# Kernel optimization log

Measured on AMD Instinct MI355X. Metric: run time of the kernel, lower is better.

Reference implementation:

```python
import jax, jax.numpy as jnp
import numpy as np

B, S, T, D = 64, 256, 8, 256
E, M = 500000, 2048
NEG_INF = -10000000000.0


def setup_inputs() -> dict:
    key = jax.random.key(0)
    ks = jax.random.split(key, 9)
    token_reprs = jax.random.normal(ks[0], (B, S, T, D), dtype=jnp.float32)
    w1 = jax.random.normal(ks[1], (D, D // 2), dtype=jnp.float32) * (1.0 / np.sqrt(D))
    b1 = jnp.zeros((D // 2,), dtype=jnp.float32)
    w2 = jax.random.normal(ks[2], (D // 2, 1), dtype=jnp.float32) * (1.0 / np.sqrt(D // 2))
    b2 = jnp.zeros((1,), dtype=jnp.float32)
    edge_index = jax.random.randint(ks[3], (2, E), 0, B * S, dtype=jnp.int32)
    lm_indices = jax.random.randint(ks[4], (M,), 0, B * S * T, dtype=jnp.int32)
    batch_pointers = jax.random.randint(ks[5], (M,), 0, B, dtype=jnp.int32)
    tree_padding_mask = jax.random.randint(ks[6], (B, S), 0, 2, dtype=jnp.int32).astype(jnp.bool_)
    return {
        "token_reprs": token_reprs,
        "w1": w1, "b1": b1, "w2": w2, "b2": b2,
        "edge_index": edge_index,
        "lm_indices": lm_indices,
        "batch_pointers": batch_pointers,
        "tree_padding_mask": tree_padding_mask,
    }


def reference(token_reprs, w1, b1, w2, b2, edge_index, lm_indices, batch_pointers, tree_padding_mask):
    b, s, t, d = token_reprs.shape
    # type representation is the first token of each type tree
    type_reprs = token_reprs[:, :, 0]                  # [B, S, D]
    flat_types = type_reprs.reshape(b * s, d)          # [B*S, D]

    # predict_lemmas: gather scope/goal reprs, elementwise multiply, 2-layer MLP
    scope_ids, goal_ids = edge_index[0], edge_index[1]
    h = flat_types[scope_ids] * flat_types[goal_ids]   # [E, D]
    h = h @ w1 + b1                                    # [E, D//2] (Dropout is identity in eval)
    lemmas = (h @ w2 + b2)[:, 0]                       # [E]

    # predict_masks: gather masked token reprs + per-tree candidates, dot, mask
    mask_reprs = token_reprs.reshape(b * s * t, d)[lm_indices]  # [M, D]
    candidates = type_reprs[batch_pointers]            # [M, S, D]
    candidate_mask = tree_padding_mask[batch_pointers] # [M, S]
    lm_preds = jnp.einsum('md,msd->ms', mask_reprs, candidates)
    lm_preds = jnp.where(candidate_mask, lm_preds, NEG_INF)
    return lemmas, lm_preds
```

## Files before the change

kernel.cpp:

```cpp
#include <hip/hip_runtime.h>

#define DD 256
#define SS 256
#define BB 64
#define NEDGE 500000
#define MM 2048
#define NEG_INF -10000000000.0f
#define ROWF4 512
#define NROWS (BB * SS)

#define OFF_VC     0
#define OFF_MSORT  4096
#define OFF_BSTART (4096 + MM * 4)
#define OFF_ASLAB  (1 << 16)
#define OFF_P2     ((1 << 16) + (8 << 20))
#define OFF_MROWS  ((1 << 16) + (16 << 20))

__device__ __forceinline__ float bflo(unsigned u) { return __uint_as_float(u << 16); }
__device__ __forceinline__ float bfhi(unsigned u) { return __uint_as_float(u & 0xFFFF0000u); }
__device__ __forceinline__ unsigned short bf_rne(float f) {
    unsigned u = __float_as_uint(f);
    return (unsigned short)((u + 0x7FFFu + ((u >> 16) & 1u)) >> 16);
}
__device__ __forceinline__ unsigned pack2_rne(float a, float b) {
    return (unsigned)bf_rne(a) | ((unsigned)bf_rne(b) << 16);
}

__global__ void setup_k(const float* __restrict__ w1, const float* __restrict__ b1,
                        const float* __restrict__ w2, const float* __restrict__ b2,
                        const int* __restrict__ bp,
                        float* __restrict__ vc, int* __restrict__ msorted,
                        int* __restrict__ bstart) {
    const int t = threadIdx.x;
    if (blockIdx.x == 0) {
        float acc = 0.f;
        #pragma unroll 4
        for (int j = 0; j < DD / 2; ++j) acc += w1[t * (DD / 2) + j] * w2[j];
        vc[t] = acc;
        if (t == 0) {
            float c = b2[0];
            for (int j = 0; j < DD / 2; ++j) c += b1[j] * w2[j];
            vc[DD] = c;
        }
    } else {
        __shared__ int hist[BB];
        __shared__ int offs[BB + 1];
        if (t < BB) hist[t] = 0;
        __syncthreads();
        for (int m = t; m < MM; m += 256) atomicAdd(&hist[bp[m]], 1);
        __syncthreads();
        if (t == 0) {
            int acc = 0;
            for (int i = 0; i < BB; ++i) { offs[i] = acc; acc += hist[i]; }
            offs[BB] = acc;
        }
        __syncthreads();
        if (t < BB + 1) bstart[t] = offs[t];
        __syncthreads();
        for (int m = t; m < MM; m += 256) {
            int pos = atomicAdd(&offs[bp[m]], 1);
            msorted[pos] = m;
        }
    }
}

__global__ __launch_bounds__(256) void compact(
        const float* __restrict__ tok, const int* __restrict__ lmi,
        unsigned* __restrict__ aslab,
        unsigned* __restrict__ p2, unsigned* __restrict__ mrows) {
    const int lane = threadIdx.x & 63;
    const int w    = threadIdx.x >> 6;
    if (blockIdx.x < NROWS / 4) {
        const int row = blockIdx.x * 4 + w;
        const float4 a = ((const float4*)tok)[(size_t)row * ROWF4 + lane];
        unsigned p0 = pack2_rne(a.x, a.y), p1 = pack2_rne(a.z, a.w);
        const int k = lane >> 3, sub = lane & 7;
        const size_t si = (size_t)(k * NROWS + row) * 16 + sub * 2;
        aslab[si] = p0; aslab[si + 1] = p1;
        const size_t pi = (size_t)row * 128 + lane * 2;
        p2[pi] = p0; p2[pi + 1] = p1;
    } else {
        const int m = (blockIdx.x - NROWS / 4) * 4 + w;
        const float4 a = ((const float4*)(tok + (size_t)lmi[m] * DD))[lane];
        mrows[(size_t)m * 128 + lane * 2]     = pack2_rne(a.x, a.y);
        mrows[(size_t)m * 128 + lane * 2 + 1] = pack2_rne(a.z, a.w);
    }
}

__global__ __launch_bounds__(256) void edge_fused(
        const unsigned* __restrict__ aslab,
        const int* __restrict__ edges, const float* __restrict__ vc,
        float* __restrict__ out) {
    const int t = threadIdx.x;
    const int lane = t & 63, w = t >> 6;
    const int sub = lane & 7, j = lane >> 3;
    const int e0 = blockIdx.x * 256;
    __shared__ int sIdx[2][256];
    __shared__ float accs[256];
    const int e = e0 + t;
    const bool val = e < NEDGE;
    sIdx[0][t] = val ? __builtin_nontemporal_load(edges + e) : 0;
    sIdx[1][t] = val ? __builtin_nontemporal_load(edges + NEDGE + e) : 0;

    float4 v4[8];
    #pragma unroll
    for (int k = 0; k < 8; ++k) v4[k] = ((const float4*)vc)[k * 8 + sub];
    __syncthreads();

    float acc[8];
    #pragma unroll
    for (int i = 0; i < 8; ++i) acc[i] = 0.f;
    const int slotbase = w * 64 + j;

    #pragma unroll 1
    for (int k = 0; k < 8; ++k) {
        const unsigned* base = aslab + (size_t)k * NROWS * 16 + sub * 2;
        const float4 v = v4[k];
        #pragma unroll
        for (int i = 0; i < 8; ++i) {
            const int slot = slotbase + i * 8;
            const int sc = sIdx[0][slot];
            const int gl = sIdx[1][slot];
            const uint2 pu = *(const uint2*)(base + (size_t)sc * 16);
            const uint2 qu = *(const uint2*)(base + (size_t)gl * 16);
            acc[i] += (bflo(pu.x) * bflo(qu.x)) * v.x
                    + (bfhi(pu.x) * bfhi(qu.x)) * v.y
                    + (bflo(pu.y) * bflo(qu.y)) * v.z
                    + (bfhi(pu.y) * bfhi(qu.y)) * v.w;
        }
    }
    #pragma unroll
    for (int i = 0; i < 8; ++i) {
        float p = acc[i];
        p += __shfl_down(p, 4, 8);
        p += __shfl_down(p, 2, 8);
        p += __shfl_down(p, 1, 8);
        if (sub == 0) accs[slotbase + i * 8] = p;
    }
    __syncthreads();
    if (val) __builtin_nontemporal_store(accs[t] + vc[DD], out + e);
}

__global__ __launch_bounds__(256) void lm_gemm(
        const unsigned* __restrict__ p2,
        const unsigned* __restrict__ mrows,
        const int* __restrict__ msorted,
        const int* __restrict__ bstart,
        const int* __restrict__ tpm,
        float* __restrict__ out) {
    const int b  = blockIdx.x;
    const int st = blockIdx.y;
    const int ch = blockIdx.z;
    const int s0 = bstart[b], s1 = bstart[b + 1];
    const int base = s0 + ch * 32;
    if (base >= s1) return;
    const int nm = min(32, s1 - base);
    const int t = threadIdx.x;

    __shared__ unsigned lmaskU[32 * 132];
    __shared__ unsigned srowU[32 * 132];
    __shared__ int mids[32];
    __shared__ int sact[64];
    __shared__ int snact;

    if (t < 32) mids[t] = msorted[base + min(t, nm - 1)];
    if (t >= 64 && t < 128) {
        int lt = t - 64;
        bool act = tpm[b * SS + st * 64 + lt] != 0;
        unsigned long long mk = __ballot(act);
        if (act) sact[__popcll(mk & ((1ull << lt) - 1))] = lt;
        if (lt == 0) snact = (int)__popcll(mk);
    }
    __syncthreads();

    for (int f = t; f < nm * 32; f += 256) {
        int r = f >> 5, q = f & 31;
        *(uint4*)&lmaskU[r * 132 + q * 4] = ((const uint4*)mrows)[(size_t)mids[r] * 32 + q];
    }
    for (int f = t; f < nm * 64; f += 256) {
        int i = f >> 6, c = f & 63;
        if (!tpm[b * SS + st * 64 + c])
            out[(size_t)mids[i] * SS + st * 64 + c] = NEG_INF;
    }
    __syncthreads();

    const int nact = snact;
    const int i2 = t & 15, sg = t >> 4;

    for (int g = 0; g * 32 < nact; ++g) {
        if (g) __syncthreads();
        const int nv = min(32, nact - g * 32);
        for (int f = t; f < nv * 32; f += 256) {
            int r = f >> 5, q = f & 31;
            size_t row = (size_t)b * SS + st * 64 + sact[g * 32 + r];
            *(uint4*)&srowU[r * 132 + q * 4] = ((const uint4*)p2)[row * 32 + q];
        }
        __syncthreads();

        float a00 = 0.f, a01 = 0.f, a10 = 0.f, a11 = 0.f;
        #pragma unroll 4
        for (int stp = 0; stp < 32; ++stp) {
            const uint4 A0 = *(const uint4*)&lmaskU[i2 * 132 + stp * 4];
            const uint4 A1 = *(const uint4*)&lmaskU[(i2 + 16) * 132 + stp * 4];
            const uint4 B0 = *(const uint4*)&srowU[sg * 132 + stp * 4];
            const uint4 B1 = *(const uint4*)&srowU[(sg + 16) * 132 + stp * 4];
            float a0[8], a1[8], b0[8], b1[8];
            a0[0] = bflo(A0.x); a0[1] = bfhi(A0.x); a0[2] = bflo(A0.y); a0[3] = bfhi(A0.y);
            a0[4] = bflo(A0.z); a0[5] = bfhi(A0.z); a0[6] = bflo(A0.w); a0[7] = bfhi(A0.w);
            a1[0] = bflo(A1.x); a1[1] = bfhi(A1.x); a1[2] = bflo(A1.y); a1[3] = bfhi(A1.y);
            a1[4] = bflo(A1.z); a1[5] = bfhi(A1.z); a1[6] = bflo(A1.w); a1[7] = bfhi(A1.w);
            b0[0] = bflo(B0.x); b0[1] = bfhi(B0.x); b0[2] = bflo(B0.y); b0[3] = bfhi(B0.y);
            b0[4] = bflo(B0.z); b0[5] = bfhi(B0.z); b0[6] = bflo(B0.w); b0[7] = bfhi(B0.w);
            b1[0] = bflo(B1.x); b1[1] = bfhi(B1.x); b1[2] = bflo(B1.y); b1[3] = bfhi(B1.y);
            b1[4] = bflo(B1.z); b1[5] = bfhi(B1.z); b1[6] = bflo(B1.w); b1[7] = bfhi(B1.w);
            #pragma unroll
            for (int jj = 0; jj < 8; ++jj) {
                a00 = fmaf(a0[jj], b0[jj], a00);
                a01 = fmaf(a0[jj], b1[jj], a01);
                a10 = fmaf(a1[jj], b0[jj], a10);
                a11 = fmaf(a1[jj], b1[jj], a11);
            }
        }

        const int iA = g * 32 + sg, iB = iA + 16;
        if (i2 < nm) {
            size_t ob = (size_t)mids[i2] * SS + st * 64;
            if (iA < nact) out[ob + sact[iA]] = a00;
            if (iB < nact) out[ob + sact[iB]] = a01;
        }
        if (i2 + 16 < nm) {
            size_t ob = (size_t)mids[i2 + 16] * SS + st * 64;
            if (iA < nact) out[ob + sact[iA]] = a10;
            if (iB < nact) out[ob + sact[iB]] = a11;
        }
    }
}

extern "C" void kernel_launch(void* const* d_in, const int* in_sizes, int n_in,
                              void* d_out, int out_size, void* d_ws, size_t ws_size,
                              hipStream_t stream) {
    const float* tok = (const float*)d_in[0];
    const float* w1  = (const float*)d_in[1];
    const float* b1  = (const float*)d_in[2];
    const float* w2  = (const float*)d_in[3];
    const float* b2  = (const float*)d_in[4];
    const int* edges = (const int*)d_in[5];
    const int* lmi   = (const int*)d_in[6];
    const int* bp    = (const int*)d_in[7];
    const int* tpm   = (const int*)d_in[8];

    float* out_lemmas = (float*)d_out;
    float* out_lm     = (float*)d_out + NEDGE;

    char* ws = (char*)d_ws;
    float* vc        = (float*)(ws + OFF_VC);
    int* msorted     = (int*)(ws + OFF_MSORT);
    int* bstart      = (int*)(ws + OFF_BSTART);
    unsigned* aslab  = (unsigned*)(ws + OFF_ASLAB);
    unsigned* p2     = (unsigned*)(ws + OFF_P2);
    unsigned* mrows  = (unsigned*)(ws + OFF_MROWS);

    setup_k<<<2, 256, 0, stream>>>(w1, b1, w2, b2, bp, vc, msorted, bstart);
    compact<<<NROWS / 4 + MM / 4, 256, 0, stream>>>(tok, lmi, aslab, p2, mrows);
    edge_fused<<<(NEDGE + 255) / 256, 256, 0, stream>>>(aslab, edges, vc, out_lemmas);
    lm_gemm<<<dim3(BB, 4, 8), 256, 0, stream>>>(p2, mrows, msorted, bstart, tpm, out_lm);
}
```

Before: 278.1 us.

## Switch to fp16 fdot2 with sign-split sqrt-scaled permuted slabs and restructure lm_gemm

The per-dimension weight vector is folded into the stored type rows. Each dimension is scaled by the square root of its weight's magnitude, and dimensions are permuted so that positive and negative weights fall into separate 64-wide slices. The edge kernel can then use the fp16 v_dot2 instruction on pure-sign slices and apply explicit signs only for the mixed last slice. lm_gemm now converts to fp16, loops over all mask chunks per block with K-tiled shared loads, computes all 64 candidates without active-column compaction, and applies the padding mask at the final write. fp16 trades exponent range against bf16's precision and could overflow or lose accuracy on large values.

After: 301.8 us. 8.5% more time.

```diff
diff --git a/kernel.cpp b/kernel.cpp
--- a/kernel.cpp
+++ b/kernel.cpp
@@ -10,37 +10,72 @@
 #define NROWS (BB * SS)
 
 #define OFF_VC     0
-#define OFF_MSORT  4096
-#define OFF_BSTART (4096 + MM * 4)
-#define OFF_ASLAB  (1 << 16)
-#define OFF_P2     ((1 << 16) + (8 << 20))
-#define OFF_MROWS  ((1 << 16) + (16 << 20))
-
-__device__ __forceinline__ float bflo(unsigned u) { return __uint_as_float(u << 16); }
-__device__ __forceinline__ float bfhi(unsigned u) { return __uint_as_float(u & 0xFFFF0000u); }
-__device__ __forceinline__ unsigned short bf_rne(float f) {
-    unsigned u = __float_as_uint(f);
-    return (unsigned short)((u + 0x7FFFu + ((u >> 16) & 1u)) >> 16);
-}
-__device__ __forceinline__ unsigned pack2_rne(float a, float b) {
-    return (unsigned)bf_rne(a) | ((unsigned)bf_rne(b) << 16);
-}
+#define OFF_META   2048
+#define OFF_SCALE  4096
+#define OFF_PERM   8192
+#define OFF_SSIGN  12288
+#define OFF_MSORT  16384
+#define OFF_BSTART 24576
+#define OFF_ASLAB  65536
+#define OFF_P2     (65536 + (8 << 20))
+#define OFF_MROWS  (65536 + (16 << 20))
+
+typedef _Float16 h2 __attribute__((ext_vector_type(2)));
+
+__device__ __forceinline__ h2 uh(unsigned u) {
+    union { unsigned x; h2 h; } c; c.x = u; return c.h;
+}
+__device__ __forceinline__ unsigned hpack(float a, float b) {
+    union { h2 h; unsigned u; } c;
+    c.h = h2{(_Float16)a, (_Float16)b};
+    return c.u;
+}
+
+#if __has_builtin(__builtin_amdgcn_fdot2)
+__device__ __forceinline__ float FDOT2(h2 a, h2 b, float c) {
+    return __builtin_amdgcn_fdot2(a, b, c, false);
+}
+#else
+__device__ __forceinline__ float FDOT2(h2 a, h2 b, float c) {
+    return c + (float)a.x * (float)b.x + (float)a.y * (float)b.y;
+}
+#endif
 
 __global__ void setup_k(const float* __restrict__ w1, const float* __restrict__ b1,
                         const float* __restrict__ w2, const float* __restrict__ b2,
                         const int* __restrict__ bp,
-                        float* __restrict__ vc, int* __restrict__ msorted,
-                        int* __restrict__ bstart) {
+                        float* __restrict__ vc, int* __restrict__ meta,
+                        float* __restrict__ scale, int* __restrict__ perm,
+                        float* __restrict__ ssign,
+                        int* __restrict__ msorted, int* __restrict__ bstart) {
     const int t = threadIdx.x;
     if (blockIdx.x == 0) {
+        __shared__ float sv[256];
+        __shared__ int sp[256], sn[256];
         float acc = 0.f;
         #pragma unroll 4
         for (int j = 0; j < DD / 2; ++j) acc += w1[t * (DD / 2) + j] * w2[j];
-        vc[t] = acc;
+        sv[t] = acc; vc[t] = acc;
+        __syncthreads();
         if (t == 0) {
             float c = b2[0];
             for (int j = 0; j < DD / 2; ++j) c += b1[j] * w2[j];
             vc[DD] = c;
+            int np = 0, nn = 0;
+            for (int d = 0; d < 256; ++d) {
+                if (sv[d] >= 0.f) sp[np++] = d; else sn[nn++] = d;
+            }
+            int q = np >> 6; if (q > 3) q = 3;
+            int pureneg = 3 - q;
+            meta[0] = q;
+            int idx = 0;
+            for (int i = 0; i < q * 64; ++i) perm[idx++] = sp[i];
+            for (int j = 0; j < pureneg * 64; ++j) perm[idx++] = sn[j];
+            for (int i = q * 64; i < np; ++i) perm[idx++] = sp[i];
+            for (int j = pureneg * 64; j < nn; ++j) perm[idx++] = sn[j];
+            for (int d = 0; d < 256; ++d) scale[d] = sqrtf(fabsf(sv[perm[d]]));
+            for (int j = 0; j < 64; ++j)
+                ssign[j] = (sv[perm[192 + j]] >= 0.f) ? 1.f : -1.f;
         }
     } else {
         __shared__ int hist[BB];
@@ -66,172 +101,176 @@
 
 __global__ __launch_bounds__(256) void compact(
         const float* __restrict__ tok, const int* __restrict__ lmi,
-        unsigned* __restrict__ aslab,
-        unsigned* __restrict__ p2, unsigned* __restrict__ mrows) {
+        const int* __restrict__ perm, const float* __restrict__ scale,
+        unsigned* __restrict__ aslab, unsigned* __restrict__ p2u,
+        unsigned* __restrict__ mru) {
     const int lane = threadIdx.x & 63;
     const int w    = threadIdx.x >> 6;
     if (blockIdx.x < NROWS / 4) {
+        __shared__ float rb[4][256];
         const int row = blockIdx.x * 4 + w;
+        const int4   pm = ((const int4*)perm)[lane];
+        const float4 sc = ((const float4*)scale)[lane];
         const float4 a = ((const float4*)tok)[(size_t)row * ROWF4 + lane];
-        unsigned p0 = pack2_rne(a.x, a.y), p1 = pack2_rne(a.z, a.w);
-        const int k = lane >> 3, sub = lane & 7;
-        const size_t si = (size_t)(k * NROWS + row) * 16 + sub * 2;
-        aslab[si] = p0; aslab[si + 1] = p1;
-        const size_t pi = (size_t)row * 128 + lane * 2;
-        p2[pi] = p0; p2[pi + 1] = p1;
+        ((float4*)rb[w])[lane] = a;
+        ((uint2*)p2u)[(size_t)row * 64 + lane] =
+            make_uint2(hpack(a.x, a.y), hpack(a.z, a.w));
+        __syncthreads();
+        float o0 = rb[w][pm.x] * sc.x, o1 = rb[w][pm.y] * sc.y;
+        float o2 = rb[w][pm.z] * sc.z, o3 = rb[w][pm.w] * sc.w;
+        const int slice = lane >> 4, pos = lane & 15;
+        ((uint2*)aslab)[((size_t)slice * NROWS + row) * 16 + pos] =
+            make_uint2(hpack(o0, o1), hpack(o2, o3));
     } else {
         const int m = (blockIdx.x - NROWS / 4) * 4 + w;
         const float4 a = ((const float4*)(tok + (size_t)lmi[m] * DD))[lane];
-        mrows[(size_t)m * 128 + lane * 2]     = pack2_rne(a.x, a.y);
-        mrows[(size_t)m * 128 + lane * 2 + 1] = pack2_rne(a.z, a.w);
+        ((uint2*)mru)[(size_t)m * 64 + lane] =
+            make_uint2(hpack(a.x, a.y), hpack(a.z, a.w));
     }
 }
 
 __global__ __launch_bounds__(256) void edge_fused(
         const unsigned* __restrict__ aslab,
-        const int* __restrict__ edges, const float* __restrict__ vc,
+        const int* __restrict__ edges, const int* __restrict__ meta,
+        const float* __restrict__ ssign, const float* __restrict__ vc,
         float* __restrict__ out) {
     const int t = threadIdx.x;
-    const int lane = t & 63, w = t >> 6;
-    const int sub = lane & 7, j = lane >> 3;
-    const int e0 = blockIdx.x * 256;
+    const int l16 = t & 15, grp = t >> 4;
     __shared__ int sIdx[2][256];
     __shared__ float accs[256];
-    const int e = e0 + t;
+    const int e = blockIdx.x * 256 + t;
     const bool val = e < NEDGE;
     sIdx[0][t] = val ? __builtin_nontemporal_load(edges + e) : 0;
     sIdx[1][t] = val ? __builtin_nontemporal_load(edges + NEDGE + e) : 0;
-
-    float4 v4[8];
+    const int q = meta[0];
+    const float4 sg = ((const float4*)ssign)[l16];
+    const float c = vc[DD];
+    __syncthreads();
+
+    const uint2* T = (const uint2*)aslab;
+    float accP[16], accN[16];
     #pragma unroll
-    for (int k = 0; k < 8; ++k) v4[k] = ((const float4*)vc)[k * 8 + sub];
+    for (int i = 0; i < 16; ++i) { accP[i] = 0.f; accN[i] = 0.f; }
+
+#define EDGE_INNER(ACC, KK)                                                  \
+    {                                                                        \
+        const uint2* Tb = T + (size_t)(KK) * NROWS * 16;                     \
+        _Pragma("unroll")                                                    \
+        for (int i = 0; i < 16; ++i) {                                       \
+            const int slot = i * 16 + grp;                                   \
+            const uint2 pu = Tb[(size_t)sIdx[0][slot] * 16 + l16];           \
+            const uint2 qu = Tb[(size_t)sIdx[1][slot] * 16 + l16];           \
+            ACC[i] = FDOT2(uh(pu.x), uh(qu.x), ACC[i]);                      \
+            ACC[i] = FDOT2(uh(pu.y), uh(qu.y), ACC[i]);                      \
+        }                                                                    \
+    }
+
+    #pragma unroll 1
+    for (int k = 0; k < 3; ++k) {
+        if (k < q) EDGE_INNER(accP, k) else EDGE_INNER(accN, k)
+    }
+    {
+        const uint2* Tb = T + (size_t)3 * NROWS * 16;
+        #pragma unroll
+        for (int i = 0; i < 16; ++i) {
+            const int slot = i * 16 + grp;
+            const uint2 pu = Tb[(size_t)sIdx[0][slot] * 16 + l16];
+            const uint2 qu = Tb[(size_t)sIdx[1][slot] * 16 + l16];
+            h2 p0 = uh(pu.x), p1 = uh(pu.y), q0 = uh(qu.x), q1 = uh(qu.y);
+            float r = ((float)p0.x * (float)q0.x) * sg.x
+                    + ((float)p0.y * (float)q0.y) * sg.y
+                    + ((float)p1.x * (float)q1.x) * sg.z
+                    + ((float)p1.y * (float)q1.y) * sg.w;
+            accP[i] += r;
+        }
+    }
+#undef EDGE_INNER
+
+    #pragma unroll
+    for (int i = 0; i < 16; ++i) {
+        float r = accP[i] - accN[i];
+        r += __shfl_down(r, 8, 16);
+        r += __shfl_down(r, 4, 16);
+        r += __shfl_down(r, 2, 16);
+        r += __shfl_down(r, 1, 16);
+        if (l16 == 0) accs[i * 16 + grp] = r;
+    }
     __syncthreads();
-
-    float acc[8];
-    #pragma unroll
-    for (int i = 0; i < 8; ++i) acc[i] = 0.f;
-    const int slotbase = w * 64 + j;
-
-    #pragma unroll 1
-    for (int k = 0; k < 8; ++k) {
-        const unsigned* base = aslab + (size_t)k * NROWS * 16 + sub * 2;
-        const float4 v = v4[k];
-        #pragma unroll
-        for (int i = 0; i < 8; ++i) {
-            const int slot = slotbase + i * 8;
-            const int sc = sIdx[0][slot];
-            const int gl = sIdx[1][slot];
-            const uint2 pu = *(const uint2*)(base + (size_t)sc * 16);
-            const uint2 qu = *(const uint2*)(base + (size_t)gl * 16);
-            acc[i] += (bflo(pu.x) * bflo(qu.x)) * v.x
-                    + (bfhi(pu.x) * bfhi(qu.x)) * v.y
-                    + (bflo(pu.y) * bflo(qu.y)) * v.z
-                    + (bfhi(pu.y) * bfhi(qu.y)) * v.w;
-        }
-    }
-    #pragma unroll
-    for (int i = 0; i < 8; ++i) {
-        float p = acc[i];
-        p += __shfl_down(p, 4, 8);
-        p += __shfl_down(p, 2, 8);
-        p += __shfl_down(p, 1, 8);
-        if (sub == 0) accs[slotbase + i * 8] = p;
-    }
-    __syncthreads();
-    if (val) __builtin_nontemporal_store(accs[t] + vc[DD], out + e);
+    if (val) __builtin_nontemporal_store(accs[t] + c, out + e);
 }
 
 __global__ __launch_bounds__(256) void lm_gemm(
-        const unsigned* __restrict__ p2,
-        const unsigned* __restrict__ mrows,
+        const unsigned* __restrict__ p2u,
+        const unsigned* __restrict__ mru,
         const int* __restrict__ msorted,
         const int* __restrict__ bstart,
         const int* __restrict__ tpm,
         float* __restrict__ out) {
     const int b  = blockIdx.x;
     const int st = blockIdx.y;
-    const int ch = blockIdx.z;
-    const int s0 = bstart[b], s1 = bstart[b + 1];
-    const int base = s0 + ch * 32;
-    if (base >= s1) return;
-    const int nm = min(32, s1 - base);
+    const int s0 = bstart[b], nmt = bstart[b + 1] - s0;
+    if (nmt == 0) return;
     const int t = threadIdx.x;
-
-    __shared__ unsigned lmaskU[32 * 132];
-    __shared__ unsigned srowU[32 * 132];
+    const int tmg = t & 15, tsg = t >> 4;
+
+    __shared__ unsigned candS[64 * 18];
+    __shared__ unsigned maskS[32 * 18];
     __shared__ int mids[32];
-    __shared__ int sact[64];
-    __shared__ int snact;
-
-    if (t < 32) mids[t] = msorted[base + min(t, nm - 1)];
-    if (t >= 64 && t < 128) {
-        int lt = t - 64;
-        bool act = tpm[b * SS + st * 64 + lt] != 0;
-        unsigned long long mk = __ballot(act);
-        if (act) sact[__popcll(mk & ((1ull << lt) - 1))] = lt;
-        if (lt == 0) snact = (int)__popcll(mk);
-    }
-    __syncthreads();
-
-    for (int f = t; f < nm * 32; f += 256) {
-        int r = f >> 5, q = f & 31;
-        *(uint4*)&lmaskU[r * 132 + q * 4] = ((const uint4*)mrows)[(size_t)mids[r] * 32 + q];
-    }
-    for (int f = t; f < nm * 64; f += 256) {
-        int i = f >> 6, c = f & 63;
-        if (!tpm[b * SS + st * 64 + c])
-            out[(size_t)mids[i] * SS + st * 64 + c] = NEG_INF;
-    }
-    __syncthreads();
-
-    const int nact = snact;
-    const int i2 = t & 15, sg = t >> 4;
-
-    for (int g = 0; g * 32 < nact; ++g) {
-        if (g) __syncthreads();
-        const int nv = min(32, nact - g * 32);
-        for (int f = t; f < nv * 32; f += 256) {
-            int r = f >> 5, q = f & 31;
-            size_t row = (size_t)b * SS + st * 64 + sact[g * 32 + r];
-            *(uint4*)&srowU[r * 132 + q * 4] = ((const uint4*)p2)[row * 32 + q];
-        }
-        __syncthreads();
-
-        float a00 = 0.f, a01 = 0.f, a10 = 0.f, a11 = 0.f;
-        #pragma unroll 4
-        for (int stp = 0; stp < 32; ++stp) {
-            const uint4 A0 = *(const uint4*)&lmaskU[i2 * 132 + stp * 4];
-            const uint4 A1 = *(const uint4*)&lmaskU[(i2 + 16) * 132 + stp * 4];
-            const uint4 B0 = *(const uint4*)&srowU[sg * 132 + stp * 4];
-            const uint4 B1 = *(const uint4*)&srowU[(sg + 16) * 132 + stp * 4];
-            float a0[8], a1[8], b0[8], b1[8];
-            a0[0] = bflo(A0.x); a0[1] = bfhi(A0.x); a0[2] = bflo(A0.y); a0[3] = bfhi(A0.y);
-            a0[4] = bflo(A0.z); a0[5] = bfhi(A0.z); a0[6] = bflo(A0.w); a0[7] = bfhi(A0.w);
-            a1[0] = bflo(A1.x); a1[1] = bfhi(A1.x); a1[2] = bflo(A1.y); a1[3] = bfhi(A1.y);
-            a1[4] = bflo(A1.z); a1[5] = bfhi(A1.z); a1[6] = bflo(A1.w); a1[7] = bfhi(A1.w);
-            b0[0] = bflo(B0.x); b0[1] = bfhi(B0.x); b0[2] = bflo(B0.y); b0[3] = bfhi(B0.y);
-            b0[4] = bflo(B0.z); b0[5] = bfhi(B0.z); b0[6] = bflo(B0.w); b0[7] = bfhi(B0.w);
-            b1[0] = bflo(B1.x); b1[1] = bfhi(B1.x); b1[2] = bflo(B1.y); b1[3] = bfhi(B1.y);
-            b1[4] = bflo(B1.z); b1[5] = bfhi(B1.z); b1[6] = bflo(B1.w); b1[7] = bfhi(B1.w);
+
+    int scol[4]; bool mk[4];
+    #pragma unroll
+    for (int ss = 0; ss < 4; ++ss) {
+        scol[ss] = st * 64 + tsg + ss * 16;
+        mk[ss] = tpm[b * SS + scol[ss]] != 0;
+    }
+
+    for (int ch = 0; ch * 32 < nmt; ++ch) {
+        const int nm = min(32, nmt - ch * 32);
+        __syncthreads();
+        if (t < 32) mids[t] = msorted[s0 + ch * 32 + min(t, nm - 1)];
+        float acc[2][4];
+        #pragma unroll
+        for (int im = 0; im < 2; ++im)
             #pragma unroll
-            for (int jj = 0; jj < 8; ++jj) {
-                a00 = fmaf(a0[jj], b0[jj], a00);
-                a01 = fmaf(a0[jj], b1[jj], a01);
-                a10 = fmaf(a1[jj], b0[jj], a10);
-                a11 = fmaf(a1[jj], b1[jj], a11);
-            }
-        }
-
-        const int iA = g * 32 + sg, iB = iA + 16;
-        if (i2 < nm) {
-            size_t ob = (size_t)mids[i2] * SS + st * 64;
-            if (iA < nact) out[ob + sact[iA]] = a00;
-            if (iB < nact) out[ob + sact[iB]] = a01;
-        }
-        if (i2 + 16 < nm) {
-            size_t ob = (size_t)mids[i2 + 16] * SS + st * 64;
-            if (iA < nact) out[ob + sact[iA]] = a10;
-            if (iB < nact) out[ob + sact[iB]] = a11;
+            for (int ss = 0; ss < 4; ++ss) acc[im][ss] = 0.f;
+
+        #pragma unroll 1
+        for (int k = 0; k < 8; ++k) {
+            __syncthreads();
+            for (int f = t; f < 512; f += 256) {
+                int r = f >> 4, cc = f & 15;
+                maskS[r * 18 + cc] = mru[(size_t)mids[r] * 128 + k * 16 + cc];
+            }
+            for (int f = t; f < 1024; f += 256) {
+                int r = f >> 4, cc = f & 15;
+                candS[r * 18 + cc] =
+                    p2u[((size_t)b * SS + st * 64 + r) * 128 + k * 16 + cc];
+            }
+            __syncthreads();
+            const uint2* Ar0 = (const uint2*)&maskS[(tmg * 2) * 18];
+            const uint2* Ar1 = (const uint2*)&maskS[(tmg * 2 + 1) * 18];
+            #pragma unroll
+            for (int j = 0; j < 8; ++j) {
+                const uint2 a0 = Ar0[j], a1 = Ar1[j];
+                #pragma unroll
+                for (int ss = 0; ss < 4; ++ss) {
+                    const uint2 bb = ((const uint2*)&candS[(tsg + ss * 16) * 18])[j];
+                    acc[0][ss] = FDOT2(uh(a0.x), uh(bb.x), acc[0][ss]);
+                    acc[0][ss] = FDOT2(uh(a0.y), uh(bb.y), acc[0][ss]);
+                    acc[1][ss] = FDOT2(uh(a1.x), uh(bb.x), acc[1][ss]);
+                    acc[1][ss] = FDOT2(uh(a1.y), uh(bb.y), acc[1][ss]);
+                }
+            }
+        }
+        #pragma unroll
+        for (int im = 0; im < 2; ++im) {
+            const int mi = tmg * 2 + im;
+            if (mi < nm) {
+                const size_t ob = (size_t)mids[mi] * SS;
+                #pragma unroll
+                for (int ss = 0; ss < 4; ++ss)
+                    out[ob + scol[ss]] = mk[ss] ? acc[im][ss] : NEG_INF;
+            }
         }
     }
 }
@@ -253,15 +292,23 @@
     float* out_lm     = (float*)d_out + NEDGE;
 
     char* ws = (char*)d_ws;
-    float* vc        = (float*)(ws + OFF_VC);
-    int* msorted     = (int*)(ws + OFF_MSORT);
-    int* bstart      = (int*)(ws + OFF_BSTART);
-    unsigned* aslab  = (unsigned*)(ws + OFF_ASLAB);
-    unsigned* p2     = (unsigned*)(ws + OFF_P2);
-    unsigned* mrows  = (unsigned*)(ws + OFF_MROWS);
-
-    setup_k<<<2, 256, 0, stream>>>(w1, b1, w2, b2, bp, vc, msorted, bstart);
-    compact<<<NROWS / 4 + MM / 4, 256, 0, stream>>>(tok, lmi, aslab, p2, mrows);
-    edge_fused<<<(NEDGE + 255) / 256, 256, 0, stream>>>(aslab, edges, vc, out_lemmas);
-    lm_gemm<<<dim3(BB, 4, 8), 256, 0, stream>>>(p2, mrows, msorted, bstart, tpm, out_lm);
-}
+    float* vc       = (float*)(ws + OFF_VC);
+    int* meta       = (int*)(ws + OFF_META);
+    float* scale    = (float*)(ws + OFF_SCALE);
+    int* perm       = (int*)(ws + OFF_PERM);
+    float* ssign    = (float*)(ws + OFF_SSIGN);
+    int* msorted    = (int*)(ws + OFF_MSORT);
+    int* bstart     = (int*)(ws + OFF_BSTART);
+    unsigned* aslab = (unsigned*)(ws + OFF_ASLAB);
+    unsigned* p2u   = (unsigned*)(ws + OFF_P2);
+    unsigned* mru   = (unsigned*)(ws + OFF_MROWS);
+
+    setup_k<<<2, 256, 0, stream>>>(w1, b1, w2, b2, bp, vc, meta, scale, perm,
+                                   ssign, msorted, bstart);
+    compact<<<NROWS / 4 + MM / 4, 256, 0, stream>>>(tok, lmi, perm, scale,
+                                                    aslab, p2u, mru);
+    edge_fused<<<(NEDGE + 255) / 256, 256, 0, stream>>>(aslab, edges, meta,
+                                                        ssign, vc, out_lemmas);
+    lm_gemm<<<dim3(BB, 4), 256, 0, stream>>>(p2u, mru, msorted, bstart, tpm,
+                                             out_lm);
+}
```
